# Performance work log

Measured on AMD Instinct MI355X. Metric: run time of the kernel, lower is better.

The kernel has to match this reference:

```python
import jax, jax.numpy as jnp
import numpy as np

N_NODES = 50000
N_EDGES = 400000
N_GRAPHS = 512
NF = 64      # node_features
EF = 32      # edge_features (RBF bins)
AIF = 92     # atom_input_features
FC = 128     # fc_features
L = 3        # conv layers
EPS = 1e-5   # BatchNorm eps


def _bn(x, gamma, beta):
    # BatchNorm1d, training-mode statistics over the batch (edge/node) dim
    m = x.mean(0)
    v = x.var(0)  # biased variance, matches torch normalization
    return (x - m) * jax.lax.rsqrt(v + EPS) * gamma + beta


def _rbf(d):
    # RBFExpansion(vmin=0, vmax=8, bins=EF): gamma = 1/mean(diff(centers))
    centers = jnp.linspace(0.0, 8.0, EF)
    gamma = 1.0 / (centers[1] - centers[0])
    return jnp.exp(-gamma * (d[:, None] - centers) ** 2)  # [E, EF]


def setup_inputs() -> dict:
    key = jax.random.key(0)
    ks = jax.random.split(key, 12)
    s = 0.05
    IN = 2 * NF + EF
    return {
        "atom_features": jax.random.normal(ks[0], (N_NODES, AIF), dtype=jnp.float32),
        "bondlength": jax.random.uniform(ks[1], (N_EDGES,), dtype=jnp.float32) * 8.0,
        "src": jax.random.randint(ks[2], (N_EDGES,), 0, N_NODES),
        "dst": jax.random.randint(ks[3], (N_EDGES,), 0, N_NODES),
        "graph_ids": jnp.sort(jax.random.randint(ks[4], (N_NODES,), 0, N_GRAPHS)),
        "W_emb": jax.random.normal(ks[5], (AIF, NF), dtype=jnp.float32) * s,
        "b_emb": jnp.zeros((NF,), jnp.float32),
        "Wi": jax.random.normal(ks[6], (L, IN, NF), dtype=jnp.float32) * s,
        "bi": jnp.zeros((L, NF), jnp.float32),
        "gi": jnp.ones((L, NF), jnp.float32),
        "bti": jnp.zeros((L, NF), jnp.float32),
        "Wu": jax.random.normal(ks[7], (L, IN, NF), dtype=jnp.float32) * s,
        "bu": jnp.zeros((L, NF), jnp.float32),
        "gu": jnp.ones((L, NF), jnp.float32),
        "btu": jnp.zeros((L, NF), jnp.float32),
        "g_bn": jnp.ones((L, NF), jnp.float32),
        "b_bn": jnp.zeros((L, NF), jnp.float32),
        "W_fc": jax.random.normal(ks[8], (NF, FC), dtype=jnp.float32) * s,
        "b_fc": jnp.zeros((FC,), jnp.float32),
        "W_out": jax.random.normal(ks[9], (FC, 1), dtype=jnp.float32) * s,
        "b_out": jnp.zeros((1,), jnp.float32),
    }


def reference(atom_features, bondlength, src, dst, graph_ids,
              W_emb, b_emb, Wi, bi, gi, bti, Wu, bu, gu, btu,
              g_bn, b_bn, W_fc, b_fc, W_out, b_out):
    e = _rbf(bondlength)                       # [E, EF]
    h = atom_features @ W_emb + b_emb          # [N, NF]
    for l in range(L):
        # gather + concat: [E, 2*NF + EF]
        z = jnp.concatenate([h[src], h[dst], e], axis=1)
        gate = jax.nn.sigmoid(_bn(z @ Wi[l] + bi[l], gi[l], bti[l]))
        upd = jax.nn.softplus(_bn(z @ Wu[l] + bu[l], gu[l], btu[l]))
        msg = gate * upd                       # [E, NF]
        agg = jax.ops.segment_sum(msg, dst, num_segments=N_NODES)
        h = jax.nn.softplus(h + _bn(agg, g_bn[l], b_bn[l]))
    # AvgPooling over nodes per graph
    counts = jax.ops.segment_sum(jnp.ones((N_NODES, 1), h.dtype), graph_ids,
                                 num_segments=N_GRAPHS)
    pooled = jax.ops.segment_sum(h, graph_ids, num_segments=N_GRAPHS)
    pooled = pooled / jnp.maximum(counts, 1.0)  # [G, NF]
    f = jax.nn.softplus(pooled)
    f = jax.nn.softplus(f @ W_fc + b_fc)
    f = jax.nn.softplus(f)
    out = f @ W_out + b_out                    # [G, 1]
    return jnp.squeeze(out)                    # [G]
```

## Files before the change

### kernel.cpp

```cpp
#include <hip/hip_runtime.h>
#include <math.h>

#define N_NODES 50000
#define N_EDGES 400000
#define N_GRAPHS 512
#define TBL 2048
#define EPSBN 1e-5f

__device__ __forceinline__ float softplusf(float x) {
  return fmaxf(x, 0.0f) + log1pf(expf(-fabsf(x)));
}
__device__ __forceinline__ float sigmoidf(float x) {
  return 1.0f / (1.0f + expf(-x));
}
__device__ __forceinline__ void fma4(float4& acc, float s, const float4& w) {
  acc.x = fmaf(s, w.x, acc.x);
  acc.y = fmaf(s, w.y, acc.y);
  acc.z = fmaf(s, w.z, acc.z);
  acc.w = fmaf(s, w.w, acc.w);
}

__global__ void k_hist(const int* __restrict__ dst, int* __restrict__ deg) {
  const int e = blockIdx.x * blockDim.x + threadIdx.x;
  if (e < N_EDGES) atomicAdd(&deg[dst[e]], 1);
}

__global__ void k_scan(const int* __restrict__ deg, int* __restrict__ rowptr,
                       int* __restrict__ cursor) {
  __shared__ int ssum[1024];
  const int t = threadIdx.x;
  const int strip = (N_NODES + 1023) / 1024;
  const int a = t * strip;
  const int b = min(N_NODES, a + strip);
  int s = 0;
  for (int i = a; i < b; ++i) s += deg[i];
  ssum[t] = s;
  __syncthreads();
  if (t == 0) {
    int run = 0;
    for (int i = 0; i < 1024; ++i) {
      const int x = ssum[i];
      ssum[i] = run;
      run += x;
    }
    rowptr[N_NODES] = run;
  }
  __syncthreads();
  int run = ssum[t];
  for (int i = a; i < b; ++i) {
    rowptr[i] = run;
    cursor[i] = run;
    run += deg[i];
  }
}

__global__ void k_scatter(const int* __restrict__ src, const int* __restrict__ dst,
                          const float* __restrict__ bond,
                          int* __restrict__ cursor,
                          int* __restrict__ csr_src, float* __restrict__ csr_f) {
  const int e = blockIdx.x * blockDim.x + threadIdx.x;
  if (e >= N_EDGES) return;
  const int d2 = dst[e];
  const int pos = atomicAdd(&cursor[d2], 1);
  csr_src[pos] = src[e];
  float f = bond[e] * ((float)(TBL - 1) / 8.0f);
  csr_f[pos] = fminf(fmaxf(f, 0.0f), (float)(TBL - 1));
}

__global__ void k_emb(const float* __restrict__ atom,
                      const float* __restrict__ Wemb,
                      const float* __restrict__ bemb,
                      float* __restrict__ h) {
  __shared__ float sW[92 * 64];
  __shared__ float sA[32 * 92];
  const int tid = threadIdx.x;
  for (int i = tid; i < 92 * 64; i += 256) sW[i] = Wemb[i];
  const int t0 = blockIdx.x * 32;
  const int nt = min(32, N_NODES - t0);
  {
    const float* srcp = atom + (size_t)t0 * 92;
    const int tot = nt * 92;
    for (int i = tid; i < tot; i += 256) sA[i] = srcp[i];
  }
  __syncthreads();
  const int col = tid & 63;
  const int ng = tid >> 6;
  const float bb = bemb[col];
  float acc[8];
#pragma unroll
  for (int i = 0; i < 8; ++i) acc[i] = bb;
  for (int kc = 0; kc < 92; kc += 4) {
    const float w0 = sW[(kc + 0) * 64 + col];
    const float w1 = sW[(kc + 1) * 64 + col];
    const float w2 = sW[(kc + 2) * 64 + col];
    const float w3 = sW[(kc + 3) * 64 + col];
#pragma unroll
    for (int i = 0; i < 8; ++i) {
      const float4 a = *(const float4*)&sA[(ng * 8 + i) * 92 + kc];
      acc[i] = fmaf(a.x, w0, acc[i]);
      acc[i] = fmaf(a.y, w1, acc[i]);
      acc[i] = fmaf(a.z, w2, acc[i]);
      acc[i] = fmaf(a.w, w3, acc[i]);
    }
  }
#pragma unroll
  for (int i = 0; i < 8; ++i) {
    const int n = t0 + ng * 8 + i;
    if (n < N_NODES) h[(size_t)n * 64 + col] = acc[i];
  }
}

__global__ void k_pq(const float* __restrict__ h,
                     const float* __restrict__ Wi_l,
                     const float* __restrict__ Wu_l,
                     float* __restrict__ PA,
                     float* __restrict__ PB) {
  __shared__ float sWA[64 * 128];
  __shared__ float sWB[64 * 128];
  __shared__ float sH[32 * 64];
  const int tid = threadIdx.x;

  for (int i = tid; i < 64 * 64; i += 256) {
    const int k = i >> 6, c = i & 63;
    sWA[k * 128 + c]      = Wi_l[k * 64 + c];
    sWA[k * 128 + 64 + c] = Wu_l[k * 64 + c];
    sWB[k * 128 + c]      = Wi_l[(64 + k) * 64 + c];
    sWB[k * 128 + 64 + c] = Wu_l[(64 + k) * 64 + c];
  }
  const int t0 = blockIdx.x * 32;
  const int nt = min(32, N_NODES - t0);
  {
    const float4* srcp = (const float4*)(h + (size_t)t0 * 64);
    const int tot4 = nt * 16;
    float4* dstp = (float4*)sH;
    for (int i = tid; i < tot4; i += 256) dstp[i] = srcp[i];
  }
  __syncthreads();

  const int wave = tid >> 6, lane = tid & 63;
  const float* wcol = (lane < 32) ? (sWA + 4 * lane) : (sWB + 4 * (lane - 32));
  const int jj = (lane < 32) ? 4 * lane : 4 * (lane - 32);
  float* OUTb = (lane < 32) ? PA : PB;

  float4 acc[8];
#pragma unroll
  for (int i = 0; i < 8; ++i) acc[i] = make_float4(0.f, 0.f, 0.f, 0.f);
  for (int kc = 0; kc < 64; kc += 4) {
    const float4 w0 = *(const float4*)(wcol + (kc + 0) * 128);
    const float4 w1 = *(const float4*)(wcol + (kc + 1) * 128);
    const float4 w2 = *(const float4*)(wcol + (kc + 2) * 128);
    const float4 w3 = *(const float4*)(wcol + (kc + 3) * 128);
#pragma unroll
    for (int i = 0; i < 8; ++i) {
      const float4 a = *(const float4*)&sH[(wave * 8 + i) * 64 + kc];
      fma4(acc[i], a.x, w0);
      fma4(acc[i], a.y, w1);
      fma4(acc[i], a.z, w2);
      fma4(acc[i], a.w, w3);
    }
  }
#pragma unroll
  for (int i = 0; i < 8; ++i) {
    const int n = t0 + wave * 8 + i;
    if (n < N_NODES) *(float4*)&OUTb[(size_t)n * 128 + jj] = acc[i];
  }
}

__global__ void k_tbl(const float* __restrict__ Wi_l,
                      const float* __restrict__ Wu_l,
                      float* __restrict__ tbl) {
  const int wave = threadIdx.x >> 6, lane = threadIdx.x & 63;
  const int t = blockIdx.x * (blockDim.x >> 6) + wave;
  if (t >= TBL) return;
  const float d = 8.0f * (float)t / (float)(TBL - 1);
  float gi_ = 0.f, gu_ = 0.f;
#pragma unroll
  for (int k = 0; k < 32; ++k) {
    const float c = 8.0f * (float)k / 31.0f;
    const float dd = d - c;
    const float r = expf(-3.875f * dd * dd);
    gi_ = fmaf(r, Wi_l[(128 + k) * 64 + lane], gi_);
    gu_ = fmaf(r, Wu_l[(128 + k) * 64 + lane], gu_);
  }
  tbl[(size_t)t * 128 + lane] = gi_;
  tbl[(size_t)t * 128 + 64 + lane] = gu_;
}

__global__ void k_edge_stats(const int* __restrict__ rowptr,
                             const int* __restrict__ csr_src,
                             const float* __restrict__ csr_f,
                             const float* __restrict__ PA,
                             const float* __restrict__ PB,
                             const float* __restrict__ tbl,
                             float* __restrict__ stats) {
  const int wave = threadIdx.x >> 6, lane = threadIdx.x & 63;
  const int wid = blockIdx.x * (blockDim.x >> 6) + wave;
  const int nw = gridDim.x * (blockDim.x >> 6);
  const float* PAj = PA + lane;
  const float* tbj = tbl + lane;
  float sg = 0.f, qg = 0.f, su = 0.f, qu = 0.f;
  for (int n = wid; n < N_NODES; n += nw) {
    const int r0 = rowptr[n], r1 = rowptr[n + 1];
    if (r0 == r1) continue;
    const float pbg = PB[(size_t)n * 128 + lane];
    const float pbu = PB[(size_t)n * 128 + 64 + lane];
    for (int k = r0; k < r1; ++k) {
      const int s = csr_src[k];
      const float cf = csr_f[k];
      const int i0 = min((int)cf, TBL - 2);
      const float fr = cf - (float)i0;
      const float* ta = tbj + (size_t)i0 * 128;
      const float pag = PAj[(size_t)s * 128];
      const float pau = PAj[(size_t)s * 128 + 64];
      const float yg = pag + pbg + fmaf(fr, ta[128] - ta[0], ta[0]);
      const float yu = pau + pbu + fmaf(fr, ta[192] - ta[64], ta[64]);
      sg += yg; qg = fmaf(yg, yg, qg);
      su += yu; qu = fmaf(yu, yu, qu);
    }
  }
  __shared__ float red[4][4][64];
  red[0][wave][lane] = sg;
  red[1][wave][lane] = qg;
  red[2][wave][lane] = su;
  red[3][wave][lane] = qu;
  __syncthreads();
  const float v = red[wave][0][lane] + red[wave][1][lane] +
                  red[wave][2][lane] + red[wave][3][lane];
  atomicAdd(&stats[wave * 64 + lane], v);
}

__global__ void k_fin_gu(const float* __restrict__ stats,
                         const float* __restrict__ gi_l, const float* __restrict__ bti_l,
                         const float* __restrict__ gu_l, const float* __restrict__ btu_l,
                         float* __restrict__ coefs) {
  const int j = threadIdx.x;
  const float invE = 1.0f / (float)N_EDGES;
  float m = stats[j] * invE;
  float v = fmaxf(stats[64 + j] * invE - m * m, 0.0f);
  float a = gi_l[j] * rsqrtf(v + EPSBN);
  coefs[j] = a;
  coefs[64 + j] = fmaf(-m, a, bti_l[j]);
  m = stats[128 + j] * invE;
  v = fmaxf(stats[192 + j] * invE - m * m, 0.0f);
  a = gu_l[j] * rsqrtf(v + EPSBN);
  coefs[128 + j] = a;
  coefs[192 + j] = fmaf(-m, a, btu_l[j]);
}

__global__ void k_edge_apply(const int* __restrict__ rowptr,
                             const int* __restrict__ csr_src,
                             const float* __restrict__ csr_f,
                             const float* __restrict__ PA,
                             float* PBm,
                             const float* __restrict__ tbl,
                             const float* __restrict__ coefs,
                             float* __restrict__ stats) {
  const int wave = threadIdx.x >> 6, lane = threadIdx.x & 63;
  const int wid = blockIdx.x * (blockDim.x >> 6) + wave;
  const int nw = gridDim.x * (blockDim.x >> 6);
  const float ag = coefs[lane], bg = coefs[64 + lane];
  const float au = coefs[128 + lane], bu = coefs[192 + lane];
  const float* PAj = PA + lane;
  const float* tbj = tbl + lane;
  float ssum = 0.f, sqsum = 0.f;
  for (int n = wid; n < N_NODES; n += nw) {
    const int r0 = rowptr[n], r1 = rowptr[n + 1];
    float msum = 0.f;
    if (r0 < r1) {
      const float pbg = PBm[(size_t)n * 128 + lane];
      const float pbu = PBm[(size_t)n * 128 + 64 + lane];
      for (int k = r0; k < r1; ++k) {
        const int s = csr_src[k];
        const float cf = csr_f[k];
        const int i0 = min((int)cf, TBL - 2);
        const float fr = cf - (float)i0;
        const float* ta = tbj + (size_t)i0 * 128;
        const float pag = PAj[(size_t)s * 128];
        const float pau = PAj[(size_t)s * 128 + 64];
        const float yg = pag + pbg + fmaf(fr, ta[128] - ta[0], ta[0]);
        const float yu = pau + pbu + fmaf(fr, ta[192] - ta[64], ta[64]);
        msum += sigmoidf(fmaf(ag, yg, bg)) * softplusf(fmaf(au, yu, bu));
      }
    }
    PBm[(size_t)n * 128 + lane] = msum;
    ssum += msum;
    sqsum = fmaf(msum, msum, sqsum);
  }
  __shared__ float red[2][4][64];
  red[0][wave][lane] = ssum;
  red[1][wave][lane] = sqsum;
  __syncthreads();
  if (wave < 2) {
    const float vv = red[wave][0][lane] + red[wave][1][lane] +
                     red[wave][2][lane] + red[wave][3][lane];
    atomicAdd(&stats[256 + wave * 64 + lane], vv);
  }
}

__global__ void k_fin_agg(const float* __restrict__ stats,
                          const float* __restrict__ gbn_l, const float* __restrict__ bbn_l,
                          float* __restrict__ coefs) {
  const int j = threadIdx.x;
  const float invN = 1.0f / (float)N_NODES;
  const float m = stats[256 + j] * invN;
  const float v = fmaxf(stats[320 + j] * invN - m * m, 0.0f);
  const float a = gbn_l[j] * rsqrtf(v + EPSBN);
  coefs[256 + j] = a;
  coefs[320 + j] = fmaf(-m, a, bbn_l[j]);
}

__global__ void k_hupd(float* __restrict__ h, const float* __restrict__ PBm,
                       const float* __restrict__ coefs) {
  const int stride = blockDim.x * gridDim.x;
  for (int i = blockIdx.x * blockDim.x + threadIdx.x; i < N_NODES * 64; i += stride) {
    const int j = i & 63;
    const int n = i >> 6;
    const float x = h[i] + fmaf(coefs[256 + j], PBm[(size_t)n * 128 + j], coefs[320 + j]);
    h[i] = softplusf(x);
  }
}

__global__ void k_pool(const float* __restrict__ h, const int* __restrict__ gid,
                       float* __restrict__ pooled, float* __restrict__ counts) {
  const int wave = threadIdx.x >> 6, lane = threadIdx.x & 63;
  const int wpb = blockDim.x >> 6;
  const int nw = wpb * gridDim.x;
  for (int n = blockIdx.x * wpb + wave; n < N_NODES; n += nw) {
    const int g = gid[n];
    atomicAdd(&pooled[(size_t)g * 64 + lane], h[(size_t)n * 64 + lane]);
    if (lane == 0) atomicAdd(&counts[g], 1.0f);
  }
}

__global__ void k_final(const float* __restrict__ pooled, const float* __restrict__ counts,
                        const float* __restrict__ Wfc, const float* __restrict__ bfc,
                        const float* __restrict__ Wout, const float* __restrict__ bout,
                        float* __restrict__ out) {
  __shared__ float f1[64];
  __shared__ float red[128];
  const int g = blockIdx.x, t = threadIdx.x;
  if (t < 64) {
    const float c = fmaxf(counts[g], 1.0f);
    f1[t] = softplusf(pooled[(size_t)g * 64 + t] / c);
  }
  __syncthreads();
  float acc = bfc[t];
#pragma unroll
  for (int k = 0; k < 64; ++k) acc = fmaf(f1[k], Wfc[k * 128 + t], acc);
  red[t] = softplusf(softplusf(acc)) * Wout[t];
  __syncthreads();
  for (int s2 = 64; s2 > 0; s2 >>= 1) {
    if (t < s2) red[t] += red[t + s2];
    __syncthreads();
  }
  if (t == 0) out[g] = red[0] + bout[0];
}

extern "C" void kernel_launch(void* const* d_in, const int* in_sizes, int n_in,
                              void* d_out, int out_size, void* d_ws, size_t ws_size,
                              hipStream_t stream) {
  const float* atom = (const float*)d_in[0];
  const float* bond = (const float*)d_in[1];
  const int* src = (const int*)d_in[2];
  const int* dst = (const int*)d_in[3];
  const int* gid = (const int*)d_in[4];
  const float* Wemb = (const float*)d_in[5];
  const float* bemb = (const float*)d_in[6];
  const float* Wi = (const float*)d_in[7];
  const float* gi = (const float*)d_in[9];
  const float* bti = (const float*)d_in[10];
  const float* Wu = (const float*)d_in[11];
  const float* gub = (const float*)d_in[13];
  const float* btu = (const float*)d_in[14];
  const float* gbn = (const float*)d_in[15];
  const float* bbn = (const float*)d_in[16];
  const float* Wfc = (const float*)d_in[17];
  const float* bfc = (const float*)d_in[18];
  const float* Wout = (const float*)d_in[19];
  const float* bout = (const float*)d_in[20];

  float* h = (float*)d_ws;
  float* PA = h + (size_t)N_NODES * 64;
  float* PB = PA + (size_t)N_NODES * 128;
  float* tbl = PB + (size_t)N_NODES * 128;
  float* stats = tbl + (size_t)TBL * 128;
  float* coefs = stats + 384;
  int* deg = (int*)(coefs + 384);
  float* pooled = (float*)(deg + N_NODES);
  float* counts = pooled + (size_t)N_GRAPHS * 64;
  int* rowptr = (int*)(counts + N_GRAPHS);
  int* cursor = rowptr + N_NODES + 1;
  int* csr_src = cursor + N_NODES;
  float* csr_f = (float*)(csr_src + N_EDGES);

  const int ntiles = (N_NODES + 31) / 32;
  const int egrid = (N_EDGES + 255) / 256;

  (void)hipMemsetAsync(deg, 0,
                       (size_t)(N_NODES + N_GRAPHS * 64 + N_GRAPHS) * 4, stream);
  k_hist<<<egrid, 256, 0, stream>>>(dst, deg);
  k_scan<<<1, 1024, 0, stream>>>(deg, rowptr, cursor);
  k_scatter<<<egrid, 256, 0, stream>>>(src, dst, bond, cursor, csr_src, csr_f);

  k_emb<<<ntiles, 256, 0, stream>>>(atom, Wemb, bemb, h);
  for (int l = 0; l < 3; ++l) {
    const float* Wi_l = Wi + (size_t)l * 160 * 64;
    const float* Wu_l = Wu + (size_t)l * 160 * 64;
    (void)hipMemsetAsync(stats, 0, 384 * sizeof(float), stream);
    k_pq<<<ntiles, 256, 0, stream>>>(h, Wi_l, Wu_l, PA, PB);
    k_tbl<<<TBL / 4, 256, 0, stream>>>(Wi_l, Wu_l, tbl);
    k_edge_stats<<<1024, 256, 0, stream>>>(rowptr, csr_src, csr_f,
                                           PA, PB, tbl, stats);
    k_fin_gu<<<1, 64, 0, stream>>>(stats, gi + l * 64, bti + l * 64,
                                   gub + l * 64, btu + l * 64, coefs);
    k_edge_apply<<<1024, 256, 0, stream>>>(rowptr, csr_src, csr_f,
                                           PA, PB, tbl, coefs, stats);
    k_fin_agg<<<1, 64, 0, stream>>>(stats, gbn + l * 64, bbn + l * 64, coefs);
    k_hupd<<<1024, 256, 0, stream>>>(h, PB, coefs);
  }
  k_pool<<<512, 256, 0, stream>>>(h, gid, pooled, counts);
  k_final<<<N_GRAPHS, 128, 0, stream>>>(pooled, counts, Wfc, bfc, Wout, bout,
                                        (float*)d_out);
}
```

Measured before the change: 1.915 ms.

## Store node projections and RBF table in fp16 to halve edge-gather traffic

The per-node projections PA and PB and the RBF interpolation table are now stored as half precision and converted to float after each load. The aim is to roughly halve the bytes moved by the random per-edge gathers in both the statistics pass and the apply pass. The table is shrunk from 2048 to 512 entries, the edge kernels launch twice as many blocks, and aggregation now writes to its own float buffer instead of overwriting PB. The cost is fp16 rounding of pre-BatchNorm activations and coarser table interpolation, which may affect accuracy.

```diff
diff --git a/kernel.cpp b/kernel.cpp
--- a/kernel.cpp
+++ b/kernel.cpp
@@ -1,10 +1,11 @@
 #include <hip/hip_runtime.h>
+#include <hip/hip_fp16.h>
 #include <math.h>
 
 #define N_NODES 50000
 #define N_EDGES 400000
 #define N_GRAPHS 512
-#define TBL 2048
+#define TBL 512
 #define EPSBN 1e-5f
 
 __device__ __forceinline__ float softplusf(float x) {
@@ -113,8 +114,8 @@
 __global__ void k_pq(const float* __restrict__ h,
                      const float* __restrict__ Wi_l,
                      const float* __restrict__ Wu_l,
-                     float* __restrict__ PA,
-                     float* __restrict__ PB) {
+                     __half* __restrict__ PA,
+                     __half* __restrict__ PB) {
   __shared__ float sWA[64 * 128];
   __shared__ float sWB[64 * 128];
   __shared__ float sH[32 * 64];
@@ -140,7 +141,7 @@
   const int wave = tid >> 6, lane = tid & 63;
   const float* wcol = (lane < 32) ? (sWA + 4 * lane) : (sWB + 4 * (lane - 32));
   const int jj = (lane < 32) ? 4 * lane : 4 * (lane - 32);
-  float* OUTb = (lane < 32) ? PA : PB;
+  __half* OUTb = (lane < 32) ? PA : PB;
 
   float4 acc[8];
 #pragma unroll
@@ -162,13 +163,20 @@
 #pragma unroll
   for (int i = 0; i < 8; ++i) {
     const int n = t0 + wave * 8 + i;
-    if (n < N_NODES) *(float4*)&OUTb[(size_t)n * 128 + jj] = acc[i];
+    if (n < N_NODES) {
+      ushort4 u;
+      u.x = __half_as_ushort(__float2half_rn(acc[i].x));
+      u.y = __half_as_ushort(__float2half_rn(acc[i].y));
+      u.z = __half_as_ushort(__float2half_rn(acc[i].z));
+      u.w = __half_as_ushort(__float2half_rn(acc[i].w));
+      *(ushort4*)&OUTb[(size_t)n * 128 + jj] = u;
+    }
   }
 }
 
 __global__ void k_tbl(const float* __restrict__ Wi_l,
                       const float* __restrict__ Wu_l,
-                      float* __restrict__ tbl) {
+                      __half* __restrict__ tbl) {
   const int wave = threadIdx.x >> 6, lane = threadIdx.x & 63;
   const int t = blockIdx.x * (blockDim.x >> 6) + wave;
   if (t >= TBL) return;
@@ -182,38 +190,40 @@
     gi_ = fmaf(r, Wi_l[(128 + k) * 64 + lane], gi_);
     gu_ = fmaf(r, Wu_l[(128 + k) * 64 + lane], gu_);
   }
-  tbl[(size_t)t * 128 + lane] = gi_;
-  tbl[(size_t)t * 128 + 64 + lane] = gu_;
+  tbl[(size_t)t * 128 + lane] = __float2half_rn(gi_);
+  tbl[(size_t)t * 128 + 64 + lane] = __float2half_rn(gu_);
 }
 
 __global__ void k_edge_stats(const int* __restrict__ rowptr,
                              const int* __restrict__ csr_src,
                              const float* __restrict__ csr_f,
-                             const float* __restrict__ PA,
-                             const float* __restrict__ PB,
-                             const float* __restrict__ tbl,
+                             const __half* __restrict__ PA,
+                             const __half* __restrict__ PB,
+                             const __half* __restrict__ tbl,
                              float* __restrict__ stats) {
   const int wave = threadIdx.x >> 6, lane = threadIdx.x & 63;
   const int wid = blockIdx.x * (blockDim.x >> 6) + wave;
   const int nw = gridDim.x * (blockDim.x >> 6);
-  const float* PAj = PA + lane;
-  const float* tbj = tbl + lane;
+  const __half* PAj = PA + lane;
+  const __half* tbj = tbl + lane;
   float sg = 0.f, qg = 0.f, su = 0.f, qu = 0.f;
   for (int n = wid; n < N_NODES; n += nw) {
     const int r0 = rowptr[n], r1 = rowptr[n + 1];
     if (r0 == r1) continue;
-    const float pbg = PB[(size_t)n * 128 + lane];
-    const float pbu = PB[(size_t)n * 128 + 64 + lane];
+    const float pbg = __half2float(PB[(size_t)n * 128 + lane]);
+    const float pbu = __half2float(PB[(size_t)n * 128 + 64 + lane]);
     for (int k = r0; k < r1; ++k) {
       const int s = csr_src[k];
       const float cf = csr_f[k];
       const int i0 = min((int)cf, TBL - 2);
       const float fr = cf - (float)i0;
-      const float* ta = tbj + (size_t)i0 * 128;
-      const float pag = PAj[(size_t)s * 128];
-      const float pau = PAj[(size_t)s * 128 + 64];
-      const float yg = pag + pbg + fmaf(fr, ta[128] - ta[0], ta[0]);
-      const float yu = pau + pbu + fmaf(fr, ta[192] - ta[64], ta[64]);
+      const __half* ta = tbj + (size_t)i0 * 128;
+      const float pag = __half2float(PAj[(size_t)s * 128]);
+      const float pau = __half2float(PAj[(size_t)s * 128 + 64]);
+      const float tg0 = __half2float(ta[0]), tg1 = __half2float(ta[128]);
+      const float tu0 = __half2float(ta[64]), tu1 = __half2float(ta[192]);
+      const float yg = pag + pbg + fmaf(fr, tg1 - tg0, tg0);
+      const float yu = pau + pbu + fmaf(fr, tu1 - tu0, tu0);
       sg += yg; qg = fmaf(yg, yg, qg);
       su += yu; qu = fmaf(yu, yu, qu);
     }
@@ -250,39 +260,42 @@
 __global__ void k_edge_apply(const int* __restrict__ rowptr,
                              const int* __restrict__ csr_src,
                              const float* __restrict__ csr_f,
-                             const float* __restrict__ PA,
-                             float* PBm,
-                             const float* __restrict__ tbl,
+                             const __half* __restrict__ PA,
+                             const __half* __restrict__ PB,
+                             const __half* __restrict__ tbl,
                              const float* __restrict__ coefs,
+                             float* __restrict__ agg,
                              float* __restrict__ stats) {
   const int wave = threadIdx.x >> 6, lane = threadIdx.x & 63;
   const int wid = blockIdx.x * (blockDim.x >> 6) + wave;
   const int nw = gridDim.x * (blockDim.x >> 6);
   const float ag = coefs[lane], bg = coefs[64 + lane];
   const float au = coefs[128 + lane], bu = coefs[192 + lane];
-  const float* PAj = PA + lane;
-  const float* tbj = tbl + lane;
+  const __half* PAj = PA + lane;
+  const __half* tbj = tbl + lane;
   float ssum = 0.f, sqsum = 0.f;
   for (int n = wid; n < N_NODES; n += nw) {
     const int r0 = rowptr[n], r1 = rowptr[n + 1];
     float msum = 0.f;
     if (r0 < r1) {
-      const float pbg = PBm[(size_t)n * 128 + lane];
-      const float pbu = PBm[(size_t)n * 128 + 64 + lane];
+      const float pbg = __half2float(PB[(size_t)n * 128 + lane]);
+      const float pbu = __half2float(PB[(size_t)n * 128 + 64 + lane]);
       for (int k = r0; k < r1; ++k) {
         const int s = csr_src[k];
         const float cf = csr_f[k];
         const int i0 = min((int)cf, TBL - 2);
         const float fr = cf - (float)i0;
-        const float* ta = tbj + (size_t)i0 * 128;
-        const float pag = PAj[(size_t)s * 128];
-        const float pau = PAj[(size_t)s * 128 + 64];
-        const float yg = pag + pbg + fmaf(fr, ta[128] - ta[0], ta[0]);
-        const float yu = pau + pbu + fmaf(fr, ta[192] - ta[64], ta[64]);
+        const __half* ta = tbj + (size_t)i0 * 128;
+        const float pag = __half2float(PAj[(size_t)s * 128]);
+        const float pau = __half2float(PAj[(size_t)s * 128 + 64]);
+        const float tg0 = __half2float(ta[0]), tg1 = __half2float(ta[128]);
+        const float tu0 = __half2float(ta[64]), tu1 = __half2float(ta[192]);
+        const float yg = pag + pbg + fmaf(fr, tg1 - tg0, tg0);
+        const float yu = pau + pbu + fmaf(fr, tu1 - tu0, tu0);
         msum += sigmoidf(fmaf(ag, yg, bg)) * softplusf(fmaf(au, yu, bu));
       }
     }
-    PBm[(size_t)n * 128 + lane] = msum;
+    agg[(size_t)n * 64 + lane] = msum;
     ssum += msum;
     sqsum = fmaf(msum, msum, sqsum);
   }
@@ -309,13 +322,12 @@
   coefs[320 + j] = fmaf(-m, a, bbn_l[j]);
 }
 
-__global__ void k_hupd(float* __restrict__ h, const float* __restrict__ PBm,
+__global__ void k_hupd(float* __restrict__ h, const float* __restrict__ agg,
                        const float* __restrict__ coefs) {
   const int stride = blockDim.x * gridDim.x;
   for (int i = blockIdx.x * blockDim.x + threadIdx.x; i < N_NODES * 64; i += stride) {
     const int j = i & 63;
-    const int n = i >> 6;
-    const float x = h[i] + fmaf(coefs[256 + j], PBm[(size_t)n * 128 + j], coefs[320 + j]);
+    const float x = h[i] + fmaf(coefs[256 + j], agg[i], coefs[320 + j]);
     h[i] = softplusf(x);
   }
 }
@@ -380,10 +392,11 @@
   const float* bout = (const float*)d_in[20];
 
   float* h = (float*)d_ws;
-  float* PA = h + (size_t)N_NODES * 64;
-  float* PB = PA + (size_t)N_NODES * 128;
-  float* tbl = PB + (size_t)N_NODES * 128;
-  float* stats = tbl + (size_t)TBL * 128;
+  float* agg = h + (size_t)N_NODES * 64;
+  __half* PA = (__half*)(agg + (size_t)N_NODES * 64);
+  __half* PB = PA + (size_t)N_NODES * 128;
+  __half* tbl = PB + (size_t)N_NODES * 128;
+  float* stats = (float*)(tbl + (size_t)TBL * 128);
   float* coefs = stats + 384;
   int* deg = (int*)(coefs + 384);
   float* pooled = (float*)(deg + N_NODES);
@@ -409,14 +422,14 @@
     (void)hipMemsetAsync(stats, 0, 384 * sizeof(float), stream);
     k_pq<<<ntiles, 256, 0, stream>>>(h, Wi_l, Wu_l, PA, PB);
     k_tbl<<<TBL / 4, 256, 0, stream>>>(Wi_l, Wu_l, tbl);
-    k_edge_stats<<<1024, 256, 0, stream>>>(rowptr, csr_src, csr_f,
+    k_edge_stats<<<2048, 256, 0, stream>>>(rowptr, csr_src, csr_f,
                                            PA, PB, tbl, stats);
     k_fin_gu<<<1, 64, 0, stream>>>(stats, gi + l * 64, bti + l * 64,
                                    gub + l * 64, btu + l * 64, coefs);
-    k_edge_apply<<<1024, 256, 0, stream>>>(rowptr, csr_src, csr_f,
-                                           PA, PB, tbl, coefs, stats);
+    k_edge_apply<<<2048, 256, 0, stream>>>(rowptr, csr_src, csr_f,
+                                           PA, PB, tbl, coefs, agg, stats);
     k_fin_agg<<<1, 64, 0, stream>>>(stats, gbn + l * 64, bbn + l * 64, coefs);
-    k_hupd<<<1024, 256, 0, stream>>>(h, PB, coefs);
+    k_hupd<<<1024, 256, 0, stream>>>(h, agg, coefs);
   }
   k_pool<<<512, 256, 0, stream>>>(h, gid, pooled, counts);
   k_final<<<N_GRAPHS, 128, 0, stream>>>(pooled, counts, Wfc, bfc, Wout, bout,
```

Result: faster. 1.868 ms (-2.5%).
